# Kernel optimization log

Hardware: AMD Instinct MI355X
Metric: run time of the kernel (lower is better)

The kernel has to match this reference:

```python
import jax, jax.numpy as jnp
import numpy as np

INPUT_DIM = 28
OUTPUT_DIM = 21
LAYER_SIZE = 64
NUM_HIDDEN = 10  # number of 64x64 hidden layers after the input layer


def setup_inputs() -> dict:
    key = jax.random.key(0)
    ks = jax.random.split(key, 7)
    x = jax.random.normal(ks[0], (1048576, INPUT_DIM), dtype=jnp.float32)
    # PyTorch nn.Linear default init: U(-1/sqrt(fan_in), 1/sqrt(fan_in)); plain uniform is fine for a baseline.
    s_in = 1.0 / np.sqrt(INPUT_DIM)
    s_h = 1.0 / np.sqrt(LAYER_SIZE)
    W_in = jax.random.uniform(ks[1], (INPUT_DIM, LAYER_SIZE), jnp.float32, -s_in, s_in)
    b_in = jax.random.uniform(ks[2], (LAYER_SIZE,), jnp.float32, -s_in, s_in)
    W_hid = jax.random.uniform(ks[3], (NUM_HIDDEN, LAYER_SIZE, LAYER_SIZE), jnp.float32, -s_h, s_h)
    b_hid = jax.random.uniform(ks[4], (NUM_HIDDEN, LAYER_SIZE), jnp.float32, -s_h, s_h)
    W_out = jax.random.uniform(ks[5], (LAYER_SIZE, OUTPUT_DIM), jnp.float32, -s_h, s_h)
    b_out = jax.random.uniform(ks[6], (OUTPUT_DIM,), jnp.float32, -s_h, s_h)
    return {"x": x, "W_in": W_in, "b_in": b_in, "W_hid": W_hid, "b_hid": b_hid,
            "W_out": W_out, "b_out": b_out}


def reference(x, W_in, b_in, W_hid, b_hid, W_out, b_out):
    h = jax.nn.relu(x @ W_in + b_in)  # [B, 64]
    def step(h, wb):
        W, b = wb
        return jax.nn.relu(h @ W + b), None
    h, _ = jax.lax.scan(step, h, (W_hid, b_hid))
    return jax.nn.sigmoid(h @ W_out + b_out)  # [B, 21]
```

## Files before the change

### kernel.cpp

```cpp
#include <hip/hip_runtime.h>

#define DEV __device__ __forceinline__

typedef _Float16 half8 __attribute__((ext_vector_type(8)));
typedef _Float16 half2v __attribute__((ext_vector_type(2)));
typedef float f32x16 __attribute__((ext_vector_type(16)));
typedef int int4v __attribute__((ext_vector_type(4)));

DEV f32x16 mfma16(half8 a, half8 b, f32x16 c) {
    return __builtin_amdgcn_mfma_f32_32x32x16_f16(a, b, c, 0, 0, 0);
}
DEV half8 h8(int4v v) { return __builtin_bit_cast(half8, v); }
DEV half8 ldh8(const _Float16* p) { return *(const half8*)p; }
DEV int pkrtz(float a, float b) {
    auto t = __builtin_amdgcn_cvt_pkrtz(a, b);
    return __builtin_bit_cast(int, t);
}
DEV int relupk(float a, float b) {
    int p = pkrtz(a, b);
    half2v h = __builtin_bit_cast(half2v, p);
    half2v z = {(_Float16)0.f, (_Float16)0.f};
    h = __builtin_elementwise_max(h, z);
    return __builtin_bit_cast(int, h);
}
DEV void plswap(int& a, int& b) {
    asm("v_permlane32_swap_b32 %0, %1" : "+v"(a), "+v"(b));
}

DEV f32x16 zero16() {
    f32x16 z = {0.f,0.f,0.f,0.f,0.f,0.f,0.f,0.f,0.f,0.f,0.f,0.f,0.f,0.f,0.f,0.f};
    return z;
}

struct Frags { int4v c[4]; };

DEV void repack(const f32x16& C0, const f32x16& C1, Frags& B) {
    int P0[8], P1[8];
#pragma unroll
    for (int q = 0; q < 8; ++q) {
        P0[q] = relupk(C0[2*q], C0[2*q+1]);
        P1[q] = relupk(C1[2*q], C1[2*q+1]);
    }
#pragma unroll
    for (int kk = 0; kk < 4; ++kk) {
        const int* Pm = (kk < 2) ? P0 : P1;
        int idx = 4 * (kk & 1);
        int a0 = Pm[idx + 0], b0 = Pm[idx + 2];
        int a1 = Pm[idx + 1], b1 = Pm[idx + 3];
        plswap(a0, b0);
        plswap(a1, b1);
        int4v nb; nb[0] = a0; nb[1] = a1; nb[2] = b0; nb[3] = b1;
        B.c[kk] = nb;
    }
}

DEV void hid_step(const _Float16* wb, int lam, int4v ones, Frags& B0, Frags& B1) {
    const _Float16* p0 = wb + lam * 8;
    const _Float16* p1 = wb + 2560 + lam * 8;
    half8 a40 = ldh8(p0 + 2048);
    half8 a41 = ldh8(p1 + 2048);
    __builtin_amdgcn_s_setprio(1);
    f32x16 C00 = mfma16(a40, h8(ones), zero16());
    f32x16 C01 = mfma16(a41, h8(ones), zero16());
    f32x16 C10 = mfma16(a40, h8(ones), zero16());
    f32x16 C11 = mfma16(a41, h8(ones), zero16());
#pragma unroll
    for (int kk = 0; kk < 4; ++kk) {
        half8 a0 = ldh8(p0 + kk * 512);
        half8 a1 = ldh8(p1 + kk * 512);
        half8 b0 = h8(B0.c[kk]);
        half8 b1 = h8(B1.c[kk]);
        C00 = mfma16(a0, b0, C00);
        C01 = mfma16(a1, b0, C01);
        C10 = mfma16(a0, b1, C10);
        C11 = mfma16(a1, b1, C11);
    }
    __builtin_amdgcn_s_setprio(0);
    repack(C00, C01, B0);
    repack(C10, C11, B1);
}

DEV void in_step(const _Float16* wb, int lam, Frags& B0, Frags& B1) {
    const _Float16* p0 = wb + lam * 8;
    const _Float16* p1 = wb + 1024 + lam * 8;
    f32x16 C00, C01, C10, C11;
    __builtin_amdgcn_s_setprio(1);
    {
        half8 a0 = ldh8(p0);
        half8 a1 = ldh8(p1);
        half8 b0 = h8(B0.c[0]);
        half8 b1 = h8(B1.c[0]);
        C00 = mfma16(a0, b0, zero16());
        C01 = mfma16(a1, b0, zero16());
        C10 = mfma16(a0, b1, zero16());
        C11 = mfma16(a1, b1, zero16());
    }
    {
        half8 a0 = ldh8(p0 + 512);
        half8 a1 = ldh8(p1 + 512);
        half8 b0 = h8(B0.c[1]);
        half8 b1 = h8(B1.c[1]);
        C00 = mfma16(a0, b0, C00);
        C01 = mfma16(a1, b0, C01);
        C10 = mfma16(a0, b1, C10);
        C11 = mfma16(a1, b1, C11);
    }
    __builtin_amdgcn_s_setprio(0);
    repack(C00, C01, B0);
    repack(C10, C11, B1);
}

DEV void out_step2(const _Float16* wb, int lam, int4v ones,
                   const Frags& B0, const Frags& B1, float* __restrict__ out, int row0, int row1) {
    const int h = lam >> 5;
    const _Float16* p = wb + lam * 8;
    half8 a4 = ldh8(p + 2048);
    __builtin_amdgcn_s_setprio(1);
    f32x16 Ca = mfma16(a4, h8(ones), zero16());
    f32x16 Cb = mfma16(a4, h8(ones), zero16());
#pragma unroll
    for (int kk = 0; kk < 4; ++kk) {
        half8 a = ldh8(p + kk * 512);
        Ca = mfma16(a, h8(B0.c[kk]), Ca);
        Cb = mfma16(a, h8(B1.c[kk]), Cb);
    }
    __builtin_amdgcn_s_setprio(0);
    float* oa = out + row0 * 21;
    float* ob = out + row1 * 21;
#pragma unroll
    for (int r = 0; r < 16; ++r) {
        int f = (r & 3) + 8 * (r >> 2) + 4 * h;
        if (f < 21) {
            oa[f] = __builtin_amdgcn_rcpf(1.f + __expf(-Ca[r]));
            ob[f] = __builtin_amdgcn_rcpf(1.f + __expf(-Cb[r]));
        }
    }
}

DEV void load_x(const float* __restrict__ x, int row, int h, Frags& B) {
    const float* xr = x + row * 28;
    float4 fa = *(const float4*)(xr + 8 * h);
    float4 fb = *(const float4*)(xr + 8 * h + 4);
    float4 fc = *(const float4*)(xr + 16 + 8 * h);
    float4 fd = (h == 0) ? *(const float4*)(xr + 20) : make_float4(1.f, 0.f, 0.f, 0.f);
    int4v c0, c1;
    c0[0] = pkrtz(fa.x, fa.y); c0[1] = pkrtz(fa.z, fa.w);
    c0[2] = pkrtz(fb.x, fb.y); c0[3] = pkrtz(fb.z, fb.w);
    c1[0] = pkrtz(fc.x, fc.y); c1[1] = pkrtz(fc.z, fc.w);
    c1[2] = pkrtz(fd.x, fd.y); c1[3] = pkrtz(fd.z, fd.w);
    B.c[0] = c0; B.c[1] = c1;
}

#define NT 1024

__global__ __attribute__((amdgpu_flat_work_group_size(NT, NT), amdgpu_waves_per_eu(4, 4)))
void mlp_fused(
    const float* __restrict__ x, const float* __restrict__ W_in, const float* __restrict__ b_in,
    const float* __restrict__ W_hid, const float* __restrict__ b_hid,
    const float* __restrict__ W_out, const float* __restrict__ b_out,
    float* __restrict__ out) {
    __shared__ __align__(16) _Float16 wH[51200];
    __shared__ __align__(16) _Float16 wI[2048];
    __shared__ __align__(16) _Float16 wO[2560];

    const int tid = threadIdx.x;

    for (int i = tid; i < 10240; i += NT) {
        int l = i >> 10, rem = i & 1023, m = rem >> 9, off = rem & 511;
        wH[l * 5120 + m * 2560 + 2048 + off] = (_Float16)0.f;
    }
    for (int i = tid; i < 2048; i += NT) wI[i] = (_Float16)0.f;
    for (int i = tid; i < 2560; i += NT) wO[i] = (_Float16)0.f;
    __syncthreads();

    for (int i = tid; i < 40960; i += NT) {
        int o = i & 63, kin = (i >> 6) & 63, l = i >> 12;
        int m = o >> 5, kk = kin >> 4, hh = (kin >> 3) & 1, e = kin & 7;
        int lam = hh * 32 + (o & 31);
        wH[l * 5120 + m * 2560 + kk * 512 + lam * 8 + e] = (_Float16)W_hid[i];
    }
    for (int i = tid; i < 640; i += NT) {
        int l = i >> 6, f = i & 63, m = f >> 5, r = f & 31;
        wH[l * 5120 + m * 2560 + 2048 + r * 8] = (_Float16)b_hid[i];
    }
    for (int i = tid; i < 1792; i += NT) {
        int o = i & 63, kin = i >> 6;
        int m = o >> 5, kk = kin >> 4, hh = (kin >> 3) & 1, e = kin & 7;
        int lam = hh * 32 + (o & 31);
        wI[m * 1024 + kk * 512 + lam * 8 + e] = (_Float16)W_in[i];
    }
    for (int i = tid; i < 64; i += NT) {
        int m = i >> 5;
        wI[m * 1024 + 512 + (32 + (i & 31)) * 8 + 4] = (_Float16)b_in[i];
    }
    for (int i = tid; i < 1344; i += NT) {
        int o = i % 21, kin = i / 21;
        int kk = kin >> 4, hh = (kin >> 3) & 1, e = kin & 7;
        int lam = hh * 32 + o;
        wO[kk * 512 + lam * 8 + e] = (_Float16)W_out[i];
    }
    for (int i = tid; i < 21; i += NT)
        wO[4 * 512 + i * 8] = (_Float16)b_out[i];
    __syncthreads();

    const int w = tid >> 6, lam = tid & 63;
    const int col = lam & 31, h = lam >> 5;
    int4v ones; ones[0] = (h == 0) ? 0x3C00 : 0; ones[1] = 0; ones[2] = 0; ones[3] = 0;

    for (int i = 0; i < w; ++i) __builtin_amdgcn_s_sleep(4);

    const int tbase = blockIdx.x * 128;
#pragma unroll 1
    for (int pb = w * 2; pb < 128; pb += 32) {
        int t0 = tbase + pb;
        int row0 = t0 * 32 + col, row1 = row0 + 32;
        Frags B0, B1;
        load_x(x, row0, h, B0);
        load_x(x, row1, h, B1);
        in_step(wI, lam, B0, B1);
        const _Float16* wp = wH;
#pragma unroll 1
        for (int l = 0; l < 10; ++l) {
            hid_step(wp, lam, ones, B0, B1);
            wp += 5120;
        }
        out_step2(wO, lam, ones, B0, B1, out, row0, row1);
    }
}

extern "C" void kernel_launch(void* const* d_in, const int* in_sizes, int n_in,
                              void* d_out, int out_size, void* d_ws, size_t ws_size,
                              hipStream_t stream) {
    const float* x     = (const float*)d_in[0];
    const float* W_in  = (const float*)d_in[1];
    const float* b_in  = (const float*)d_in[2];
    const float* W_hid = (const float*)d_in[3];
    const float* b_hid = (const float*)d_in[4];
    const float* W_out = (const float*)d_in[5];
    const float* b_out = (const float*)d_in[6];
    float* out = (float*)d_out;
    mlp_fused<<<dim3(256), dim3(NT), 0, stream>>>(x, W_in, b_in, W_hid, b_hid, W_out, b_out, out);
}
```

Baseline: 116.8 us.

## Process four 32-row tiles per wave with 512-thread blocks

Each wave now carries four 32-row batch tiles through the MLP instead of two, so every weight fragment read from LDS feeds four MFMAs per output half instead of two. To make room for the larger register footprint, the block shrinks to 512 threads and occupancy drops to 2 waves per EU. The staggered start sleep is reduced to odd waves only. Fewer concurrent waves may leave less latency hiding for the dependent MFMA chains and the repack work.

```diff
diff --git a/kernel.cpp b/kernel.cpp
--- a/kernel.cpp
+++ b/kernel.cpp
@@ -54,85 +54,87 @@
     }
 }
 
-DEV void hid_step(const _Float16* wb, int lam, int4v ones, Frags& B0, Frags& B1) {
+DEV void hid_step4(const _Float16* wb, int lam, int4v ones, const f32x16& Z, Frags* B) {
     const _Float16* p0 = wb + lam * 8;
     const _Float16* p1 = wb + 2560 + lam * 8;
     half8 a40 = ldh8(p0 + 2048);
     half8 a41 = ldh8(p1 + 2048);
+    f32x16 CA[4], CB[4];
     __builtin_amdgcn_s_setprio(1);
-    f32x16 C00 = mfma16(a40, h8(ones), zero16());
-    f32x16 C01 = mfma16(a41, h8(ones), zero16());
-    f32x16 C10 = mfma16(a40, h8(ones), zero16());
-    f32x16 C11 = mfma16(a41, h8(ones), zero16());
+#pragma unroll
+    for (int t = 0; t < 4; ++t) {
+        CA[t] = mfma16(a40, h8(ones), Z);
+        CB[t] = mfma16(a41, h8(ones), Z);
+    }
 #pragma unroll
     for (int kk = 0; kk < 4; ++kk) {
         half8 a0 = ldh8(p0 + kk * 512);
         half8 a1 = ldh8(p1 + kk * 512);
-        half8 b0 = h8(B0.c[kk]);
-        half8 b1 = h8(B1.c[kk]);
-        C00 = mfma16(a0, b0, C00);
-        C01 = mfma16(a1, b0, C01);
-        C10 = mfma16(a0, b1, C10);
-        C11 = mfma16(a1, b1, C11);
+#pragma unroll
+        for (int t = 0; t < 4; ++t) {
+            half8 bt = h8(B[t].c[kk]);
+            CA[t] = mfma16(a0, bt, CA[t]);
+            CB[t] = mfma16(a1, bt, CB[t]);
+        }
     }
     __builtin_amdgcn_s_setprio(0);
-    repack(C00, C01, B0);
-    repack(C10, C11, B1);
-}
-
-DEV void in_step(const _Float16* wb, int lam, Frags& B0, Frags& B1) {
+#pragma unroll
+    for (int t = 0; t < 4; ++t) repack(CA[t], CB[t], B[t]);
+}
+
+DEV void in_step4(const _Float16* wb, int lam, const f32x16& Z, Frags* B) {
     const _Float16* p0 = wb + lam * 8;
     const _Float16* p1 = wb + 1024 + lam * 8;
-    f32x16 C00, C01, C10, C11;
+    f32x16 CA[4], CB[4];
     __builtin_amdgcn_s_setprio(1);
     {
         half8 a0 = ldh8(p0);
         half8 a1 = ldh8(p1);
-        half8 b0 = h8(B0.c[0]);
-        half8 b1 = h8(B1.c[0]);
-        C00 = mfma16(a0, b0, zero16());
-        C01 = mfma16(a1, b0, zero16());
-        C10 = mfma16(a0, b1, zero16());
-        C11 = mfma16(a1, b1, zero16());
+#pragma unroll
+        for (int t = 0; t < 4; ++t) {
+            half8 bt = h8(B[t].c[0]);
+            CA[t] = mfma16(a0, bt, Z);
+            CB[t] = mfma16(a1, bt, Z);
+        }
     }
     {
         half8 a0 = ldh8(p0 + 512);
         half8 a1 = ldh8(p1 + 512);
-        half8 b0 = h8(B0.c[1]);
-        half8 b1 = h8(B1.c[1]);
-        C00 = mfma16(a0, b0, C00);
-        C01 = mfma16(a1, b0, C01);
-        C10 = mfma16(a0, b1, C10);
-        C11 = mfma16(a1, b1, C11);
+#pragma unroll
+        for (int t = 0; t < 4; ++t) {
+            half8 bt = h8(B[t].c[1]);
+            CA[t] = mfma16(a0, bt, CA[t]);
+            CB[t] = mfma16(a1, bt, CB[t]);
+        }
     }
     __builtin_amdgcn_s_setprio(0);
-    repack(C00, C01, B0);
-    repack(C10, C11, B1);
-}
-
-DEV void out_step2(const _Float16* wb, int lam, int4v ones,
-                   const Frags& B0, const Frags& B1, float* __restrict__ out, int row0, int row1) {
+#pragma unroll
+    for (int t = 0; t < 4; ++t) repack(CA[t], CB[t], B[t]);
+}
+
+DEV void out_step4(const _Float16* wb, int lam, int4v ones, const f32x16& Z,
+                   const Frags* B, float* __restrict__ out, const int* rows) {
     const int h = lam >> 5;
     const _Float16* p = wb + lam * 8;
     half8 a4 = ldh8(p + 2048);
+    f32x16 C[4];
     __builtin_amdgcn_s_setprio(1);
-    f32x16 Ca = mfma16(a4, h8(ones), zero16());
-    f32x16 Cb = mfma16(a4, h8(ones), zero16());
+#pragma unroll
+    for (int t = 0; t < 4; ++t) C[t] = mfma16(a4, h8(ones), Z);
 #pragma unroll
     for (int kk = 0; kk < 4; ++kk) {
         half8 a = ldh8(p + kk * 512);
-        Ca = mfma16(a, h8(B0.c[kk]), Ca);
-        Cb = mfma16(a, h8(B1.c[kk]), Cb);
+#pragma unroll
+        for (int t = 0; t < 4; ++t) C[t] = mfma16(a, h8(B[t].c[kk]), C[t]);
     }
     __builtin_amdgcn_s_setprio(0);
-    float* oa = out + row0 * 21;
-    float* ob = out + row1 * 21;
-#pragma unroll
-    for (int r = 0; r < 16; ++r) {
-        int f = (r & 3) + 8 * (r >> 2) + 4 * h;
-        if (f < 21) {
-            oa[f] = __builtin_amdgcn_rcpf(1.f + __expf(-Ca[r]));
-            ob[f] = __builtin_amdgcn_rcpf(1.f + __expf(-Cb[r]));
+#pragma unroll
+    for (int t = 0; t < 4; ++t) {
+        float* o = out + rows[t] * 21;
+#pragma unroll
+        for (int r = 0; r < 16; ++r) {
+            int f = (r & 3) + 8 * (r >> 2) + 4 * h;
+            if (f < 21) o[f] = __builtin_amdgcn_rcpf(1.f + __expf(-C[t][r]));
         }
     }
 }
@@ -151,9 +153,9 @@
     B.c[0] = c0; B.c[1] = c1;
 }
 
-#define NT 1024
-
-__global__ __attribute__((amdgpu_flat_work_group_size(NT, NT), amdgpu_waves_per_eu(4, 4)))
+#define NT 512
+
+__global__ __attribute__((amdgpu_flat_work_group_size(NT, NT), amdgpu_waves_per_eu(2, 2)))
 void mlp_fused(
     const float* __restrict__ x, const float* __restrict__ W_in, const float* __restrict__ b_in,
     const float* __restrict__ W_hid, const float* __restrict__ b_hid,
@@ -206,25 +208,30 @@
     const int w = tid >> 6, lam = tid & 63;
     const int col = lam & 31, h = lam >> 5;
     int4v ones; ones[0] = (h == 0) ? 0x3C00 : 0; ones[1] = 0; ones[2] = 0; ones[3] = 0;
-
-    for (int i = 0; i < w; ++i) __builtin_amdgcn_s_sleep(4);
+    const f32x16 Z = zero16();
+
+    if (w & 1) __builtin_amdgcn_s_sleep(13);
 
     const int tbase = blockIdx.x * 128;
 #pragma unroll 1
-    for (int pb = w * 2; pb < 128; pb += 32) {
-        int t0 = tbase + pb;
-        int row0 = t0 * 32 + col, row1 = row0 + 32;
-        Frags B0, B1;
-        load_x(x, row0, h, B0);
-        load_x(x, row1, h, B1);
-        in_step(wI, lam, B0, B1);
+    for (int j = 0; j < 4; ++j) {
+        int q = w + 8 * j;
+        int t0 = tbase + q * 4;
+        Frags B[4];
+        int rows[4];
+#pragma unroll
+        for (int t = 0; t < 4; ++t) {
+            rows[t] = (t0 + t) * 32 + col;
+            load_x(x, rows[t], h, B[t]);
+        }
+        in_step4(wI, lam, Z, B);
         const _Float16* wp = wH;
 #pragma unroll 1
         for (int l = 0; l < 10; ++l) {
-            hid_step(wp, lam, ones, B0, B1);
+            hid_step4(wp, lam, ones, Z, B);
             wp += 5120;
         }
-        out_step2(wO, lam, ones, B0, B1, out, row0, row1);
+        out_step4(wO, lam, ones, Z, B, out, rows);
     }
 }
 
```

Result: faster. 109.5 us (-6.3%).
